# Performance work log

Hardware: AMD Instinct MI355X
Metric: run time of the kernel (lower is better)

The kernel has to match this reference:

```python
import jax, jax.numpy as jnp
import numpy as np

B, S, D, H, FF = 2, 2048, 1024, 16, 4096
HD = D // H
EPS = 1e-5


def _ln(x, g, b):
    m = jnp.mean(x, axis=-1, keepdims=True)
    v = jnp.mean((x - m) ** 2, axis=-1, keepdims=True)
    return (x - m) * jax.lax.rsqrt(v + EPS) * g + b


def _rope(x, cos, sin):
    # non-standard RoPE: split full d_model at half, rotate (pre head-split)
    half = x.shape[-1] // 2
    x1, x2 = x[..., :half], x[..., half:]
    return jnp.concatenate([x1 * cos - x2 * sin, x1 * sin + x2 * cos], axis=-1)


def _heads(x, b, s):
    return x.reshape(b, s, H, HD).transpose(0, 2, 1, 3)  # [b,h,s,hd]


def _attn(q, k, v):
    scores = jnp.einsum('bhqd,bhkd->bhqk', q, k) / jnp.sqrt(jnp.float32(HD))
    w = jax.nn.softmax(scores, axis=-1)
    return jnp.einsum('bhqk,bhkd->bhqd', w, v)


def setup_inputs() -> dict:
    key = jax.random.key(0)
    ks = jax.random.split(key, 32)
    sc = 0.02
    d = {
        'x': jax.random.normal(ks[0], (B, S, D), jnp.float32),
        'cond_emb': jax.random.normal(ks[1], (B, D), jnp.float32),
    }
    # proper RoPE tables over half_dim = D//2
    pos = np.arange(S)[:, None]
    inv = 1.0 / (10000.0 ** (np.arange(D // 2) / (D // 2)))
    ang = pos * inv[None, :]
    d['cos_pos'] = jnp.asarray(np.cos(ang), jnp.float32)
    d['sin_pos'] = jnp.asarray(np.sin(ang), jnp.float32)
    names = ['Wq', 'Wk', 'Wv', 'Wo', 'Wqc', 'Wkc', 'Wvc', 'Woc']
    for i, n in enumerate(names):
        d[n] = jax.random.normal(ks[2 + i], (D, D), jnp.float32) * sc
        d['b' + n[1:]] = jnp.zeros((D,), jnp.float32)
    d['W1'] = jax.random.normal(ks[12], (D, FF), jnp.float32) * sc
    d['b1'] = jnp.zeros((FF,), jnp.float32)
    d['W2'] = jax.random.normal(ks[13], (FF, D), jnp.float32) * sc
    d['b2'] = jnp.zeros((D,), jnp.float32)
    for i in (1, 2, 3):
        d[f'g{i}'] = jnp.ones((D,), jnp.float32)
        d[f'be{i}'] = jnp.zeros((D,), jnp.float32)
    return d


def reference(x, cond_emb, cos_pos, sin_pos,
              Wq, bq, Wk, bk, Wv, bv, Wo, bo,
              Wqc, bqc, Wkc, bkc, Wvc, bvc, Woc, boc,
              W1, b1, W2, b2, g1, be1, g2, be2, g3, be3):
    b, s, _ = x.shape
    # self-attention with RoPE applied on full d_model before head split
    residual = x
    xn = _ln(x, g1, be1)
    q = _rope(xn @ Wq + bq, cos_pos, sin_pos)
    k = _rope(xn @ Wk + bk, cos_pos, sin_pos)
    v = xn @ Wv + bv
    o = _attn(_heads(q, b, s), _heads(k, b, s), _heads(v, b, s))
    o = o.transpose(0, 2, 1, 3).reshape(b, s, D) @ Wo + bo
    x = residual + o
    # cross-attention with single-token context
    residual = x
    xn = _ln(x, g2, be2)
    cond = cond_emb[:, None, :]  # [b,1,D]
    qc = _heads(xn @ Wqc + bqc, b, s)
    kc = _heads(cond @ Wkc + bkc, b, 1)
    vc = _heads(cond @ Wvc + bvc, b, 1)
    oc = _attn(qc, kc, vc)
    oc = oc.transpose(0, 2, 1, 3).reshape(b, s, D) @ Woc + boc
    x = residual + oc
    # FFN (exact GELU)
    residual = x
    xn = _ln(x, g3, be3)
    h = jax.nn.gelu(xn @ W1 + b1, approximate=False)
    return residual + (h @ W2 + b2)
```

## Files before the change

kernel.cpp:

```cpp
#include <hip/hip_runtime.h>
#include <cmath>

#define B_  2
#define S_  2048
#define D_  1024
#define H_  16
#define HD_ 64
#define FF_ 4096
#define M_  4096

typedef __attribute__((ext_vector_type(8))) __bf16 bf16x8;
typedef __attribute__((ext_vector_type(4))) __bf16 bf16x4;
typedef __attribute__((ext_vector_type(4))) float  f32x4;
typedef __attribute__((ext_vector_type(16))) float f32x16;
typedef __attribute__((ext_vector_type(4))) unsigned u32x4;

__device__ __forceinline__ void gload_lds16(void* lds, const void* g) {
    __builtin_amdgcn_global_load_lds(
        (const __attribute__((address_space(1))) unsigned int*)g,
        (__attribute__((address_space(3))) unsigned int*)lds,
        16, 0, 0);
}

#define FENCE() asm volatile("" ::: "memory")

__device__ __forceinline__ unsigned pk_bf16(float lo, float hi) {
    unsigned short lu = __builtin_bit_cast(unsigned short, (__bf16)lo);
    unsigned short hu = __builtin_bit_cast(unsigned short, (__bf16)hi);
    return (unsigned)lu | ((unsigned)hu << 16);
}

__global__ __launch_bounds__(256)
void tcast(const float* __restrict__ src, __bf16* __restrict__ dst, int K, int N)
{
    __shared__ float t[32][33];
    int tx = threadIdx.x & 31, ty = threadIdx.x >> 5;
    int k0 = blockIdx.y * 32, n0 = blockIdx.x * 32;
#pragma unroll
    for (int i = 0; i < 4; ++i)
        t[ty + i * 8][tx] = src[(size_t)(k0 + ty + i * 8) * N + n0 + tx];
    __syncthreads();
#pragma unroll
    for (int i = 0; i < 4; ++i)
        dst[(size_t)(n0 + ty + i * 8) * K + k0 + tx] = (__bf16)t[tx][ty + i * 8];
}

__global__ __launch_bounds__(256)
void tcast3(const float* __restrict__ wa, const float* __restrict__ wb,
            const float* __restrict__ wc, __bf16* __restrict__ dstb)
{
    __shared__ float t[32][33];
    const float* src = blockIdx.z == 0 ? wa : (blockIdx.z == 1 ? wb : wc);
    __bf16* dst = dstb + (size_t)blockIdx.z * 1024 * 1024;
    int tx = threadIdx.x & 31, ty = threadIdx.x >> 5;
    int k0 = blockIdx.y * 32, n0 = blockIdx.x * 32;
#pragma unroll
    for (int i = 0; i < 4; ++i)
        t[ty + i * 8][tx] = src[(size_t)(k0 + ty + i * 8) * 1024 + n0 + tx];
    __syncthreads();
#pragma unroll
    for (int i = 0; i < 4; ++i)
        dst[(size_t)(n0 + ty + i * 8) * 1024 + k0 + tx] = (__bf16)t[tx][ty + i * 8];
}

__global__ __launch_bounds__(256)
void catb(const float* __restrict__ a, const float* __restrict__ b,
          const float* __restrict__ c, float* __restrict__ o)
{
    int i = blockIdx.x * 256 + threadIdx.x;
    o[i] = i < 1024 ? a[i] : (i < 2048 ? b[i - 1024] : c[i - 2048]);
}

__global__ __launch_bounds__(256)
void colgemv(const float* __restrict__ inp, const float* __restrict__ W,
             const float* __restrict__ bias, float* __restrict__ out, int K, int N)
{
    __shared__ float part[4][16];
    const int b = blockIdx.y;
    const int t = threadIdx.x;
    const int w = t >> 6, lane = t & 63;
    const int colIdx = lane & 15;
    const int col = blockIdx.x * 16 + colIdx;
    const int ks = w * 4 + (lane >> 4);
    const int kpt = K >> 4;
    const float* ip = inp + (size_t)b * K + ks * kpt;
    const float* wp = W + (size_t)ks * kpt * N + col;
    float acc = 0.f;
#pragma unroll 8
    for (int i = 0; i < kpt; ++i)
        acc += ip[i] * wp[(size_t)i * N];
    acc += __shfl_xor(acc, 16);
    acc += __shfl_xor(acc, 32);
    if (lane < 16) part[w][colIdx] = acc;
    __syncthreads();
    if (t < 16) {
        float r = part[0][t] + part[1][t] + part[2][t] + part[3][t]
                + bias[blockIdx.x * 16 + t];
        out[(size_t)b * N + blockIdx.x * 16 + t] = r;
    }
}

__global__ __launch_bounds__(256)
void ln_cast(const float* __restrict__ x, const float* __restrict__ g,
             const float* __restrict__ be, __bf16* __restrict__ out)
{
    int row = blockIdx.x, tid = threadIdx.x;
    const float4* xp = (const float4*)(x + (size_t)row * D_);
    float4 v = xp[tid];
    float s  = v.x + v.y + v.z + v.w;
    float s2 = v.x * v.x + v.y * v.y + v.z * v.z + v.w * v.w;
#pragma unroll
    for (int off = 32; off > 0; off >>= 1) {
        s  += __shfl_down(s, off);
        s2 += __shfl_down(s2, off);
    }
    __shared__ float rs[4], rs2[4];
    int wid = tid >> 6, lane = tid & 63;
    if (lane == 0) { rs[wid] = s; rs2[wid] = s2; }
    __syncthreads();
    float tot  = rs[0] + rs[1] + rs[2] + rs[3];
    float tot2 = rs2[0] + rs2[1] + rs2[2] + rs2[3];
    float mean = tot * (1.0f / D_);
    float var  = tot2 * (1.0f / D_) - mean * mean;
    float rstd = rsqrtf(var + 1e-5f);
    float4 gv = ((const float4*)g)[tid];
    float4 bv = ((const float4*)be)[tid];
    bf16x4 ov;
    ov[0] = (__bf16)((v.x - mean) * rstd * gv.x + bv.x);
    ov[1] = (__bf16)((v.y - mean) * rstd * gv.y + bv.y);
    ov[2] = (__bf16)((v.z - mean) * rstd * gv.z + bv.z);
    ov[3] = (__bf16)((v.w - mean) * rstd * gv.w + bv.w);
    ((bf16x4*)(out + (size_t)row * D_))[tid] = ov;
}

__global__ __launch_bounds__(128)
void rope_qk(const __bf16* __restrict__ qkv, const float* __restrict__ cosp,
             const float* __restrict__ sinp, __bf16* __restrict__ Qh,
             __bf16* __restrict__ Kh)
{
    int row = blockIdx.x, tid = threadIdx.x;
    int b = row >> 11, s = row & 2047;
    float4 c  = ((const float4*)(cosp + (size_t)s * 512))[tid];
    float4 sn = ((const float4*)(sinp + (size_t)s * 512))[tid];
    int d0 = tid * 4;
    int h1 = d0 >> 6, dd = d0 & 63;
#pragma unroll
    for (int which = 0; which < 2; ++which) {
        const int off = which * 1024;
        const float scale = which ? 1.0f : 0.18033688f;
        __bf16* out = which ? Kh : Qh;
        bf16x4 a  = *(const bf16x4*)(qkv + (size_t)row * 3072 + off + tid * 4);
        bf16x4 bb = *(const bf16x4*)(qkv + (size_t)row * 3072 + off + 512 + tid * 4);
        float x1a = (float)a[0],  x1b = (float)a[1],  x1c = (float)a[2],  x1d = (float)a[3];
        float x2a = (float)bb[0], x2b = (float)bb[1], x2c = (float)bb[2], x2d = (float)bb[3];
        bf16x4 o1, o2;
        o1[0] = (__bf16)((x1a * c.x - x2a * sn.x) * scale);
        o1[1] = (__bf16)((x1b * c.y - x2b * sn.y) * scale);
        o1[2] = (__bf16)((x1c * c.z - x2c * sn.z) * scale);
        o1[3] = (__bf16)((x1d * c.w - x2d * sn.w) * scale);
        o2[0] = (__bf16)((x1a * sn.x + x2a * c.x) * scale);
        o2[1] = (__bf16)((x1b * sn.y + x2b * c.y) * scale);
        o2[2] = (__bf16)((x1c * sn.z + x2c * c.z) * scale);
        o2[3] = (__bf16)((x1d * sn.w + x2d * c.w) * scale);
        *(bf16x4*)(out + ((size_t)((b * H_ + h1) * S_ + s) * HD_) + dd) = o1;
        *(bf16x4*)(out + ((size_t)((b * H_ + h1 + 8) * S_ + s) * HD_) + dd) = o2;
    }
}

__global__ __launch_bounds__(256)
void vtrans2(const __bf16* __restrict__ qkv, __bf16* __restrict__ Vt)
{
    __shared__ __bf16 t[32][33];
    int tx = threadIdx.x & 31, ty = threadIdx.x >> 5;
    int bh = blockIdx.z;
    int b = bh >> 4, h = bh & 15;
    int s0 = blockIdx.y * 32, d0 = blockIdx.x * 32;
    __bf16* dst = Vt + (size_t)bh * HD_ * S_;
#pragma unroll
    for (int i = 0; i < 4; ++i)
        t[ty + i * 8][tx] = qkv[(size_t)(b * 2048 + s0 + ty + i * 8) * 3072
                                + 2048 + h * 64 + d0 + tx];
    __syncthreads();
#pragma unroll
    for (int i = 0; i < 4; ++i)
        dst[(size_t)(d0 + ty + i * 8) * S_ + s0 + tx] = t[tx][ty + i * 8];
}

template<int EPI>
__global__ __launch_bounds__(512)
void gemm8(const __bf16* __restrict__ A, const __bf16* __restrict__ Bt,
           const float* __restrict__ bias, __bf16* __restrict__ o0,
           __bf16* __restrict__ o1, int M, int N, int K, int klen)
{
    __shared__ __align__(16) char smem[131072];
    const int tid = threadIdx.x;
    const int wid = tid >> 6, lane = tid & 63;
    const int l15 = lane & 15, l16 = lane >> 4;
    const int wm = wid >> 2, wn = wid & 3;

    const int gx = gridDim.x;
    const int nwg = gx * gridDim.y;
    int wg = blockIdx.y * gx + blockIdx.x;
    wg = (wg & 7) * (nwg >> 3) + (wg >> 3);
    const int n0 = (wg % gx) * 256;
    const int m0 = (wg / gx) * 256;
    const int kz = blockIdx.z * klen;
    const size_t K2 = (size_t)K * 2;

    const int srow = tid >> 3;
    const int scol = ((tid & 7) * 16) ^ ((srow & 7) << 4);
    const char* gA = (const char*)A + (size_t)(m0 + srow) * K2 + (size_t)kz * 2 + scol;
    const char* gB = (const char*)Bt + (size_t)(n0 + srow) * K2 + (size_t)kz * 2 + scol;

    auto stageA = [&](int c) {
        char* d = (char*)smem + c * 32768 + wid * 1024;
        gload_lds16(d,         gA);
        gload_lds16(d + 8192,  gA + 64 * K2);
        gload_lds16(d + 16384, gA + 128 * K2);
        gload_lds16(d + 24576, gA + 192 * K2);
    };
    auto stageB = [&](int c) {
        char* d = (char*)smem + 65536 + c * 32768 + wid * 1024;
        gload_lds16(d,         gB);
        gload_lds16(d + 8192,  gB + 64 * K2);
        gload_lds16(d + 16384, gB + 128 * K2);
        gload_lds16(d + 24576, gB + 192 * K2);
    };

    const int sw = (l15 & 7) << 4;
    const int x0 = (l16 * 16) ^ sw;
    const int x1 = (64 + l16 * 16) ^ sw;
    const int aoff = (wm * 128 + l15) * 128;
    const int boff = 65536 + (wn * 64 + l15) * 128;

    f32x4 acc[8][4] = {};
    const int NT = klen >> 6;

    stageA(0); stageB(0); gA += 128; gB += 128;
    stageA(1); stageB(1); gA += 128; gB += 128;
    asm volatile("s_waitcnt vmcnt(8)" ::: "memory");
    __builtin_amdgcn_s_barrier();

    for (int t = 0; t < NT; ++t) {
        const int cur = t & 1;
        const char* sa = (const char*)smem + cur * 32768;
        const bool pf = (t + 2) < NT;

        bf16x8 af0[8], af1[8];
        bf16x8 b00, b01, b02, b03, b10, b11, b12, b13;

#pragma unroll
        for (int mi = 0; mi < 8; ++mi)
            af0[mi] = *(const bf16x8*)(sa + aoff + mi * 2048 + x0);
        b00 = *(const bf16x8*)(sa + boff + 0 * 2048 + x0);
        b01 = *(const bf16x8*)(sa + boff + 1 * 2048 + x0);
        FENCE();
        __builtin_amdgcn_s_barrier();
        __builtin_amdgcn_s_setprio(1);
#pragma unroll
        for (int mi = 0; mi < 8; ++mi) {
            acc[mi][0] = __builtin_amdgcn_mfma_f32_16x16x32_bf16(af0[mi], b00, acc[mi][0], 0, 0, 0);
            acc[mi][1] = __builtin_amdgcn_mfma_f32_16x16x32_bf16(af0[mi], b01, acc[mi][1], 0, 0, 0);
        }
        __builtin_amdgcn_s_setprio(0);

#pragma unroll
        for (int mi = 0; mi < 8; ++mi)
            af1[mi] = *(const bf16x8*)(sa + aoff + mi * 2048 + x1);
        b02 = *(const bf16x8*)(sa + boff + 2 * 2048 + x0);
        b03 = *(const bf16x8*)(sa + boff + 3 * 2048 + x0);
        FENCE();
        __builtin_amdgcn_s_barrier();
        __builtin_amdgcn_s_setprio(1);
#pragma unroll
        for (int mi = 0; mi < 8; ++mi) {
            acc[mi][2] = __builtin_amdgcn_mfma_f32_16x16x32_bf16(af0[mi], b02, acc[mi][2], 0, 0, 0);
            acc[mi][3] = __builtin_amdgcn_mfma_f32_16x16x32_bf16(af0[mi], b03, acc[mi][3], 0, 0, 0);
        }
        __builtin_amdgcn_s_setprio(0);

        b10 = *(const bf16x8*)(sa + boff + 0 * 2048 + x1);
        b11 = *(const bf16x8*)(sa + boff + 1 * 2048 + x1);
        FENCE();
        __builtin_amdgcn_s_barrier();
        if (pf) stageA(cur);
        __builtin_amdgcn_s_setprio(1);
#pragma unroll
        for (int mi = 0; mi < 8; ++mi) {
            acc[mi][0] = __builtin_amdgcn_mfma_f32_16x16x32_bf16(af1[mi], b10, acc[mi][0], 0, 0, 0);
            acc[mi][1] = __builtin_amdgcn_mfma_f32_16x16x32_bf16(af1[mi], b11, acc[mi][1], 0, 0, 0);
        }
        __builtin_amdgcn_s_setprio(0);

        b12 = *(const bf16x8*)(sa + boff + 2 * 2048 + x1);
        b13 = *(const bf16x8*)(sa + boff + 3 * 2048 + x1);
        FENCE();
        __builtin_amdgcn_s_barrier();
        if (pf) { stageB(cur); gA += 128; gB += 128; }
        __builtin_amdgcn_s_setprio(1);
#pragma unroll
        for (int mi = 0; mi < 8; ++mi) {
            acc[mi][2] = __builtin_amdgcn_mfma_f32_16x16x32_bf16(af1[mi], b12, acc[mi][2], 0, 0, 0);
            acc[mi][3] = __builtin_amdgcn_mfma_f32_16x16x32_bf16(af1[mi], b13, acc[mi][3], 0, 0, 0);
        }
        __builtin_amdgcn_s_setprio(0);
        if (pf) asm volatile("s_waitcnt vmcnt(8)" ::: "memory");
        else    asm volatile("s_waitcnt vmcnt(0)" ::: "memory");
        __builtin_amdgcn_s_barrier();
        FENCE();
    }

#pragma unroll
    for (int mi = 0; mi < 8; ++mi)
#pragma unroll
        for (int ni = 0; ni < 4; ++ni) {
            int gc = n0 + wn * 64 + ni * 16 + l15;
            float bb = (EPI == 2) ? 0.f : bias[gc];
#pragma unroll
            for (int r = 0; r < 4; ++r) {
                int gr = m0 + wm * 128 + mi * 16 + l16 * 4 + r;
                float v = acc[mi][ni][r] + bb;
                if constexpr (EPI == 0) {
                    o0[(size_t)gr * N + gc] = (__bf16)v;
                } else if constexpr (EPI == 1) {
                    o0[(size_t)gr * N + gc] =
                        (__bf16)(0.5f * v * (1.0f + erff(v * 0.70710678118f)));
                } else {
                    const size_t PSZ = (size_t)M_ * 1024;
                    __bf16* po = (blockIdx.z < 2) ? (o0 + blockIdx.z * PSZ)
                                                  : (o1 + (blockIdx.z - 2) * PSZ);
                    po[(size_t)gr * N + gc] = (__bf16)v;
                }
            }
        }
}

__global__ __launch_bounds__(256)
void ffn2_red(const __bf16* __restrict__ pA, const __bf16* __restrict__ pB,
              const float* __restrict__ x2, const float* __restrict__ b2,
              float* __restrict__ out)
{
    const size_t PSZ = (size_t)M_ * 1024;
    size_t i = ((size_t)blockIdx.x * 256 + threadIdx.x) * 8;
    bf16x8 a0 = *(const bf16x8*)(pA + i);
    bf16x8 a1 = *(const bf16x8*)(pA + PSZ + i);
    bf16x8 c0 = *(const bf16x8*)(pB + i);
    bf16x8 c1 = *(const bf16x8*)(pB + PSZ + i);
    float4 xa = *(const float4*)(x2 + i);
    float4 xb = *(const float4*)(x2 + i + 4);
    float xs[8] = {xa.x, xa.y, xa.z, xa.w, xb.x, xb.y, xb.z, xb.w};
#pragma unroll
    for (int j = 0; j < 8; ++j) {
        int col = (int)((i + j) & 1023);
        out[i + j] = xs[j] + b2[col]
                   + (float)a0[j] + (float)a1[j] + (float)c0[j] + (float)c1[j];
    }
}

__global__ __launch_bounds__(256)
void gemm_bt(const __bf16* __restrict__ A, const __bf16* __restrict__ Bt,
             const float* __restrict__ bias, const float* __restrict__ resid,
             const float* __restrict__ extra, float* __restrict__ outF,
             int M, int N, int K)
{
    __shared__ __align__(16) __bf16 As[128 * 64];
    __shared__ __align__(16) __bf16 Bs[128 * 64];
    const int tid = threadIdx.x;
    const int wid = tid >> 6, lane = tid & 63;
    const int m0 = blockIdx.y * 128, n0 = blockIdx.x * 128;
    const int wm = wid >> 1, wn = wid & 1;
    const int l15 = lane & 15, l16 = lane >> 4;

    f32x4 acc[4][4] = {};
    char* asb = (char*)As;
    char* bsb = (char*)Bs;
    const char* ag = (const char*)A;
    const char* bg = (const char*)Bt;
    const int srow = lane >> 3;
    const int scolsw = ((lane & 7) * 16) ^ (srow << 4);

    for (int k0 = 0; k0 < K; k0 += 64) {
        __syncthreads();
#pragma unroll
        for (int i = 0; i < 4; ++i) {
            int j = wid * 4 + i;
            int row = j * 8 + srow;
            gload_lds16(asb + j * 1024,
                        ag + (size_t)(m0 + row) * (K * 2) + k0 * 2 + scolsw);
        }
#pragma unroll
        for (int i = 0; i < 4; ++i) {
            int j = wid * 4 + i;
            int row = j * 8 + srow;
            gload_lds16(bsb + j * 1024,
                        bg + (size_t)(n0 + row) * (K * 2) + k0 * 2 + scolsw);
        }
        __syncthreads();

        bf16x8 af[4][2], bfr[4][2];
#pragma unroll
        for (int mi = 0; mi < 4; ++mi) {
            int row = wm * 64 + mi * 16 + l15;
            int swl = (row & 7) << 4;
#pragma unroll
            for (int kk = 0; kk < 2; ++kk)
                af[mi][kk] = *(const bf16x8*)(asb + row * 128 + ((l16 * 16 + kk * 64) ^ swl));
        }
#pragma unroll
        for (int ni = 0; ni < 4; ++ni) {
            int row = wn * 64 + ni * 16 + l15;
            int swl = (row & 7) << 4;
#pragma unroll
            for (int kk = 0; kk < 2; ++kk)
                bfr[ni][kk] = *(const bf16x8*)(bsb + row * 128 + ((l16 * 16 + kk * 64) ^ swl));
        }
#pragma unroll
        for (int mi = 0; mi < 4; ++mi)
#pragma unroll
            for (int ni = 0; ni < 4; ++ni) {
                acc[mi][ni] = __builtin_amdgcn_mfma_f32_16x16x32_bf16(af[mi][0], bfr[ni][0], acc[mi][ni], 0, 0, 0);
                acc[mi][ni] = __builtin_amdgcn_mfma_f32_16x16x32_bf16(af[mi][1], bfr[ni][1], acc[mi][ni], 0, 0, 0);
            }
    }

#pragma unroll
    for (int mi = 0; mi < 4; ++mi)
#pragma unroll
        for (int ni = 0; ni < 4; ++ni) {
            int gc = n0 + wn * 64 + ni * 16 + l15;
            float bb = bias[gc];
#pragma unroll
            for (int r = 0; r < 4; ++r) {
                int gr = m0 + wm * 64 + mi * 16 + l16 * 4 + r;
                float v = acc[mi][ni][r] + bb;
                size_t idx = (size_t)gr * N + gc;
                int b = gr >> 11;
                outF[idx] = resid[idx] + v + extra[(size_t)b * N + gc];
            }
        }
}

__global__ __launch_bounds__(256)
void attn_fwd(const __bf16* __restrict__ Qh, const __bf16* __restrict__ Kh,
              const __bf16* __restrict__ Vt, __bf16* __restrict__ O)
{
    __shared__ __align__(16) char smem[32768];
    const int tid = threadIdx.x, wid = tid >> 6, lane = tid & 63;
    const int l31 = lane & 31, hi = lane >> 5;

    const int wg = blockIdx.x;
    const int rr = wg >> 3;
    const int qb = rr & 15;
    const int bh = (wg & 7) + 8 * (rr >> 4);

    const int qg = qb * 128 + wid * 32 + l31;
    const size_t qkbase = (size_t)bh * S_ * HD_;

    bf16x8 qf[4];
    {
        const __bf16* qp = Qh + qkbase + (size_t)qg * HD_ + hi * 8;
#pragma unroll
        for (int kh = 0; kh < 4; ++kh)
            qf[kh] = *(const bf16x8*)(qp + kh * 16);
    }

    float m = -1e30f, sum = 0.f;
    f32x16 acc0 = {}, acc1 = {};

    const int srow = lane >> 3;
    const int scolsw = ((lane & 7) * 16) ^ ((srow & 7) << 4);
    const char* kg = (const char*)(Kh + qkbase);
    const char* vg = (const char*)(Vt + (size_t)bh * HD_ * S_);

    auto stage = [&](int c, int t) {
        int s0 = t * 64;
#pragma unroll
        for (int cc = 0; cc < 2; ++cc) {
            int j = wid * 2 + cc;
            int row = j * 8 + srow;
            gload_lds16(smem + c * 8192 + j * 1024,
                        kg + (size_t)(s0 + row) * 128 + scolsw);
            gload_lds16(smem + 16384 + c * 8192 + j * 1024,
                        vg + (size_t)row * (S_ * 2) + s0 * 2 + scolsw);
        }
    };

    const int swz0 = (l31 & 7) << 4;

    const int NT = S_ / 64;
    stage(0, 0);
    stage(1, 1);
    asm volatile("s_waitcnt vmcnt(4)" ::: "memory");
    __builtin_amdgcn_s_barrier();

    for (int kt = 0; kt < NT; ++kt) {
        const int cur = kt & 1;
        const char* Kl = smem + cur * 8192;
        const char* Vl = smem + 16384 + cur * 8192;

        f32x16 st0 = {}, st1 = {};
        __builtin_amdgcn_s_setprio(1);
#pragma unroll
        for (int kh = 0; kh < 4; ++kh) {
            int colb = kh * 32 + hi * 16;
            bf16x8 k0 = *(const bf16x8*)(Kl + l31 * 128 + (colb ^ swz0));
            bf16x8 k1 = *(const bf16x8*)(Kl + (32 + l31) * 128 + (colb ^ swz0));
            st0 = __builtin_amdgcn_mfma_f32_32x32x16_bf16(k0, qf[kh], st0, 0, 0, 0);
            st1 = __builtin_amdgcn_mfma_f32_32x32x16_bf16(k1, qf[kh], st1, 0, 0, 0);
        }
        __builtin_amdgcn_s_setprio(0);

        float rm = fmaxf(st0[0], st0[1]);
#pragma unroll
        for (int i = 2; i < 16; ++i) rm = fmaxf(rm, st0[i]);
#pragma unroll
        for (int i = 0; i < 16; ++i) rm = fmaxf(rm, st1[i]);
        rm = fmaxf(rm, __shfl_xor(rm, 32));
        if (!__all(rm <= m + 11.5f)) {
            float mn = fmaxf(m, rm);
            float corr = exp2f(m - mn);
            sum *= corr;
            acc0 *= corr;
            acc1 *= corr;
            m = mn;
        }
        f32x16 p0, p1;
        float rs = 0.f;
#pragma unroll
        for (int i = 0; i < 16; ++i) { p0[i] = exp2f(st0[i] - m); rs += p0[i]; }
#pragma unroll
        for (int i = 0; i < 16; ++i) { p1[i] = exp2f(st1[i] - m); rs += p1[i]; }
        rs += __shfl_xor(rs, 32);
        sum += rs;

        unsigned pw[2][4][2];
#pragma unroll
        for (int g = 0; g < 4; ++g)
#pragma unroll
            for (int u = 0; u < 2; ++u) {
                pw[0][g][u] = pk_bf16(p0[4 * g + 2 * u], p0[4 * g + 2 * u + 1]);
                pw[1][g][u] = pk_bf16(p1[4 * g + 2 * u], p1[4 * g + 2 * u + 1]);
            }

        __builtin_amdgcn_s_setprio(1);
#pragma unroll
        for (int khp = 0; khp < 4; ++khp) {
            const int s = khp >> 1, b0 = 2 * (khp & 1);
            u32x4 tw;
#pragma unroll
            for (int u = 0; u < 2; ++u) {
                unsigned a = pw[s][b0][u], b = pw[s][b0 + 1][u];
                unsigned pa = (unsigned)__shfl_xor((int)a, 32);
                unsigned pb = (unsigned)__shfl_xor((int)b, 32);
                tw[u]     = hi ? pb : a;
                tw[2 + u] = hi ? b  : pa;
            }
            bf16x8 pfrag = __builtin_bit_cast(bf16x8, tw);
            int colb = khp * 32 + hi * 16;
            bf16x8 v0 = *(const bf16x8*)(Vl + l31 * 128 + (colb ^ swz0));
            bf16x8 v1 = *(const bf16x8*)(Vl + (32 + l31) * 128 + (colb ^ swz0));
            acc0 = __builtin_amdgcn_mfma_f32_32x32x16_bf16(v0, pfrag, acc0, 0, 0, 0);
            acc1 = __builtin_amdgcn_mfma_f32_32x32x16_bf16(v1, pfrag, acc1, 0, 0, 0);
        }
        __builtin_amdgcn_s_setprio(0);

        FENCE();
        __builtin_amdgcn_s_barrier();
        if (kt + 2 < NT) {
            stage(cur, kt + 2);
            asm volatile("s_waitcnt vmcnt(4)" ::: "memory");
        } else {
            asm volatile("s_waitcnt vmcnt(0)" ::: "memory");
        }
        __builtin_amdgcn_s_barrier();
        FENCE();
    }

    float inv = 1.0f / sum;
    int b = bh >> 4, hh = bh & 15;
    __bf16* op = O + ((size_t)(b * S_ + qg) * D_) + hh * HD_;
#pragma unroll
    for (int ds = 0; ds < 2; ++ds) {
        f32x16 a = ds ? acc1 : acc0;
#pragma unroll
        for (int g = 0; g < 4; ++g) {
            bf16x4 ov;
#pragma unroll
            for (int e = 0; e < 4; ++e)
                ov[e] = (__bf16)(a[4 * g + e] * inv);
            *(bf16x4*)(op + ds * 32 + g * 8 + hi * 4) = ov;
        }
    }
}

extern "C" void kernel_launch(void* const* d_in, const int* in_sizes, int n_in,
                              void* d_out, int out_size, void* d_ws, size_t ws_size,
                              hipStream_t stream)
{
    (void)in_sizes; (void)n_in; (void)out_size; (void)ws_size;
    const float* x    = (const float*)d_in[0];
    const float* cond = (const float*)d_in[1];
    const float* cosp = (const float*)d_in[2];
    const float* sinp = (const float*)d_in[3];
    const float* Wq = (const float*)d_in[4];  const float* bq = (const float*)d_in[5];
    const float* Wk = (const float*)d_in[6];  const float* bk = (const float*)d_in[7];
    const float* Wv = (const float*)d_in[8];  const float* bv = (const float*)d_in[9];
    const float* Wo = (const float*)d_in[10]; const float* bo = (const float*)d_in[11];
    const float* Wvc = (const float*)d_in[16]; const float* bvc = (const float*)d_in[17];
    const float* Woc = (const float*)d_in[18]; const float* boc = (const float*)d_in[19];
    const float* W1 = (const float*)d_in[20]; const float* b1 = (const float*)d_in[21];
    const float* W2 = (const float*)d_in[22]; const float* b2 = (const float*)d_in[23];
    const float* g1 = (const float*)d_in[24]; const float* be1 = (const float*)d_in[25];
    const float* g3 = (const float*)d_in[28]; const float* be3 = (const float*)d_in[29];

    char* ws = (char*)d_ws;
    const size_t MB = 1ull << 20;
    __bf16* WqkvT = (__bf16*)(ws + 0 * MB);
    __bf16* WoT   = (__bf16*)(ws + 6 * MB);
    __bf16* W1T   = (__bf16*)(ws + 8 * MB);
    __bf16* W2T   = (__bf16*)(ws + 16 * MB);
    __bf16* xn    = (__bf16*)(ws + 24 * MB);
    __bf16* qkvh  = (__bf16*)(ws + 32 * MB);
    __bf16* Qh    = (__bf16*)(ws + 56 * MB);
    __bf16* Kh    = (__bf16*)(ws + 64 * MB);
    __bf16* Vt    = (__bf16*)(ws + 72 * MB);
    __bf16* oflat = (__bf16*)(ws + 80 * MB);
    float*  bqkv  = (float*)(ws + 88 * MB);
    float*  vc    = (float*)(ws + 88 * MB + 16384);
    float*  ocp   = (float*)(ws + 88 * MB + 32768);
    float*  x2    = (float*)(ws + 32 * MB);
    __bf16* hbuf  = (__bf16*)(ws + 48 * MB);
    __bf16* pA    = (__bf16*)(ws + 0 * MB);
    __bf16* pB    = (__bf16*)(ws + 80 * MB);

    tcast3<<<dim3(32, 32, 3), 256, 0, stream>>>(Wq, Wk, Wv, WqkvT);
    tcast<<<dim3(32, 32),  256, 0, stream>>>(Wo, WoT, 1024, 1024);
    tcast<<<dim3(128, 32), 256, 0, stream>>>(W1, W1T, 1024, 4096);
    tcast<<<dim3(32, 128), 256, 0, stream>>>(W2, W2T, 4096, 1024);
    catb<<<12, 256, 0, stream>>>(bq, bk, bv, bqkv);
    colgemv<<<dim3(64, 2), 256, 0, stream>>>(cond, Wvc, bvc, vc, 1024, 1024);
    colgemv<<<dim3(64, 2), 256, 0, stream>>>(vc, Woc, boc, ocp, 1024, 1024);
    ln_cast<<<M_, 256, 0, stream>>>(x, g1, be1, xn);
    gemm8<0><<<dim3(12, 16, 1), 512, 0, stream>>>(xn, WqkvT, bqkv, qkvh, nullptr,
                                                  M_, 3072, 1024, 1024);
    rope_qk<<<M_, 128, 0, stream>>>(qkvh, cosp, sinp, Qh, Kh);
    vtrans2<<<dim3(2, 64, 32), 256, 0, stream>>>(qkvh, Vt);
    attn_fwd<<<512, 256, 0, stream>>>(Qh, Kh, Vt, oflat);
    gemm_bt<<<dim3(8, 32), 256, 0, stream>>>(oflat, WoT, bo, x, ocp, x2,
                                             M_, 1024, 1024);
    ln_cast<<<M_, 256, 0, stream>>>(x2, g3, be3, xn);
    gemm8<1><<<dim3(16, 16, 1), 512, 0, stream>>>(xn, W1T, b1, hbuf, nullptr,
                                                  M_, 4096, 1024, 1024);
    gemm8<2><<<dim3(4, 16, 4), 512, 0, stream>>>(hbuf, W2T, nullptr, pA, pB,
                                                 M_, 1024, 4096, 1024);
    ffn2_red<<<2048, 256, 0, stream>>>(pA, pB, x2, b2, (float*)d_out);
}
```

Measured before the change: 287.4 us.

## Split attention over KV halves and merge partials with log-sum-exp

The attention kernel now splits the key sequence into two halves, launching twice as many workgroups, each writing a normalized partial output and a log-sum-exp value to workspace. A new merge kernel combines the two partials using their LSE weights into the flat output layout. The aim is more parallelism on the device (512 workgroups was few for the CU count). The cost is an extra kernel launch and round trip through memory for the partials. The row max and sum reductions are also restructured as trees to shorten dependency chains.

Result: no change. 292.4 us (+1.7%).

```diff
diff --git a/kernel.cpp b/kernel.cpp
--- a/kernel.cpp
+++ b/kernel.cpp
@@ -442,7 +442,8 @@
 
 __global__ __launch_bounds__(256)
 void attn_fwd(const __bf16* __restrict__ Qh, const __bf16* __restrict__ Kh,
-              const __bf16* __restrict__ Vt, __bf16* __restrict__ O)
+              const __bf16* __restrict__ Vt, __bf16* __restrict__ Op,
+              float* __restrict__ Lp)
 {
     __shared__ __align__(16) char smem[32768];
     const int tid = threadIdx.x, wid = tid >> 6, lane = tid & 63;
@@ -451,7 +452,9 @@
     const int wg = blockIdx.x;
     const int rr = wg >> 3;
     const int qb = rr & 15;
-    const int bh = (wg & 7) + 8 * (rr >> 4);
+    const int split = (rr >> 4) & 1;
+    const int bh = (wg & 7) + 8 * (rr >> 5);
+    const int kt0 = split * 16;
 
     const int qg = qb * 128 + wid * 32 + l31;
     const size_t qkbase = (size_t)bh * S_ * HD_;
@@ -487,14 +490,15 @@
 
     const int swz0 = (l31 & 7) << 4;
 
-    const int NT = S_ / 64;
-    stage(0, 0);
-    stage(1, 1);
+    const int NT = 16;
+    stage(0, kt0);
+    stage(1, kt0 + 1);
     asm volatile("s_waitcnt vmcnt(4)" ::: "memory");
     __builtin_amdgcn_s_barrier();
 
-    for (int kt = 0; kt < NT; ++kt) {
-        const int cur = kt & 1;
+    for (int ki = 0; ki < NT; ++ki) {
+        const int kt = kt0 + ki;
+        const int cur = ki & 1;
         const char* Kl = smem + cur * 8192;
         const char* Vl = smem + 16384 + cur * 8192;
 
@@ -510,11 +514,14 @@
         }
         __builtin_amdgcn_s_setprio(0);
 
-        float rm = fmaxf(st0[0], st0[1]);
-#pragma unroll
-        for (int i = 2; i < 16; ++i) rm = fmaxf(rm, st0[i]);
-#pragma unroll
-        for (int i = 0; i < 16; ++i) rm = fmaxf(rm, st1[i]);
+        float t16[16];
+#pragma unroll
+        for (int i = 0; i < 16; ++i) t16[i] = fmaxf(st0[i], st1[i]);
+#pragma unroll
+        for (int i = 0; i < 8; ++i) t16[i] = fmaxf(t16[i], t16[i + 8]);
+#pragma unroll
+        for (int i = 0; i < 4; ++i) t16[i] = fmaxf(t16[i], t16[i + 4]);
+        float rm = fmaxf(fmaxf(t16[0], t16[1]), fmaxf(t16[2], t16[3]));
         rm = fmaxf(rm, __shfl_xor(rm, 32));
         if (!__all(rm <= m + 11.5f)) {
             float mn = fmaxf(m, rm);
@@ -525,11 +532,18 @@
             m = mn;
         }
         f32x16 p0, p1;
-        float rs = 0.f;
-#pragma unroll
-        for (int i = 0; i < 16; ++i) { p0[i] = exp2f(st0[i] - m); rs += p0[i]; }
-#pragma unroll
-        for (int i = 0; i < 16; ++i) { p1[i] = exp2f(st1[i] - m); rs += p1[i]; }
+#pragma unroll
+        for (int i = 0; i < 16; ++i) p0[i] = exp2f(st0[i] - m);
+#pragma unroll
+        for (int i = 0; i < 16; ++i) p1[i] = exp2f(st1[i] - m);
+        float s16[16];
+#pragma unroll
+        for (int i = 0; i < 16; ++i) s16[i] = p0[i] + p1[i];
+#pragma unroll
+        for (int i = 0; i < 8; ++i) s16[i] += s16[i + 8];
+#pragma unroll
+        for (int i = 0; i < 4; ++i) s16[i] += s16[i + 4];
+        float rs = (s16[0] + s16[1]) + (s16[2] + s16[3]);
         rs += __shfl_xor(rs, 32);
         sum += rs;
 
@@ -566,7 +580,7 @@
 
         FENCE();
         __builtin_amdgcn_s_barrier();
-        if (kt + 2 < NT) {
+        if (ki + 2 < NT) {
             stage(cur, kt + 2);
             asm volatile("s_waitcnt vmcnt(4)" ::: "memory");
         } else {
@@ -577,8 +591,7 @@
     }
 
     float inv = 1.0f / sum;
-    int b = bh >> 4, hh = bh & 15;
-    __bf16* op = O + ((size_t)(b * S_ + qg) * D_) + hh * HD_;
+    __bf16* ob = Op + ((size_t)split * 65536 + (size_t)bh * 2048 + qg) * 64;
 #pragma unroll
     for (int ds = 0; ds < 2; ++ds) {
         f32x16 a = ds ? acc1 : acc0;
@@ -588,9 +601,37 @@
 #pragma unroll
             for (int e = 0; e < 4; ++e)
                 ov[e] = (__bf16)(a[4 * g + e] * inv);
-            *(bf16x4*)(op + ds * 32 + g * 8 + hi * 4) = ov;
-        }
-    }
+            *(bf16x4*)(ob + ds * 32 + g * 8 + hi * 4) = ov;
+        }
+    }
+    if (hi == 0)
+        Lp[(size_t)split * 65536 + (size_t)bh * 2048 + qg] = m + log2f(sum);
+}
+
+__global__ __launch_bounds__(256)
+void attn_merge(const __bf16* __restrict__ Op, const float* __restrict__ Lp,
+                __bf16* __restrict__ O)
+{
+    int idx = blockIdx.x * 256 + threadIdx.x;
+    int bh = idx >> 14;
+    int rem = idx & 16383;
+    int s = rem >> 3;
+    int d0 = (rem & 7) * 8;
+    size_t qi = (size_t)bh * 2048 + s;
+    float L1 = Lp[qi], L2 = Lp[65536 + qi];
+    float Lm = fmaxf(L1, L2);
+    float w1 = exp2f(L1 - Lm), w2 = exp2f(L2 - Lm);
+    float inv = 1.0f / (w1 + w2);
+    w1 *= inv; w2 *= inv;
+    bf16x8 o1 = *(const bf16x8*)(Op + qi * 64 + d0);
+    bf16x8 o2 = *(const bf16x8*)(Op + (size_t)65536 * 64 + qi * 64 + d0);
+    int b = bh >> 4, h = bh & 15;
+    __bf16* op = O + ((size_t)(b * S_ + s) * D_) + h * 64 + d0;
+    bf16x8 ov;
+#pragma unroll
+    for (int j = 0; j < 8; ++j)
+        ov[j] = (__bf16)(w1 * (float)o1[j] + w2 * (float)o2[j]);
+    *(bf16x8*)op = ov;
 }
 
 extern "C" void kernel_launch(void* const* d_in, const int* in_sizes, int n_in,
@@ -628,6 +669,8 @@
     float*  bqkv  = (float*)(ws + 88 * MB);
     float*  vc    = (float*)(ws + 88 * MB + 16384);
     float*  ocp   = (float*)(ws + 88 * MB + 32768);
+    __bf16* Opart = (__bf16*)(ws + 32 * MB);
+    float*  Lpart = (float*)(ws + 48 * MB);
     float*  x2    = (float*)(ws + 32 * MB);
     __bf16* hbuf  = (__bf16*)(ws + 48 * MB);
     __bf16* pA    = (__bf16*)(ws + 0 * MB);
@@ -645,7 +688,8 @@
                                                   M_, 3072, 1024, 1024);
     rope_qk<<<M_, 128, 0, stream>>>(qkvh, cosp, sinp, Qh, Kh);
     vtrans2<<<dim3(2, 64, 32), 256, 0, stream>>>(qkvh, Vt);
-    attn_fwd<<<512, 256, 0, stream>>>(Qh, Kh, Vt, oflat);
+    attn_fwd<<<1024, 256, 0, stream>>>(Qh, Kh, Vt, Opart, Lpart);
+    attn_merge<<<2048, 256, 0, stream>>>(Opart, Lpart, oflat);
     gemm_bt<<<dim3(8, 32), 256, 0, stream>>>(oflat, WoT, bo, x, ocp, x2,
                                              M_, 1024, 1024);
     ln_cast<<<M_, 256, 0, stream>>>(x2, g3, be3, xn);
```
